# Performance work log

Hardware: AMD Instinct MI355X
Metric: run time of the kernel (lower is better)

## Reference

```python
import jax, jax.numpy as jnp
import numpy as np

B, SQ, SK, D, H = 4, 2048, 2048, 1024, 16
HD = D // H


def setup_inputs() -> dict:
    key = jax.random.key(0)
    ks = jax.random.split(key, 8)
    s = 1.0 / np.sqrt(D)
    return {
        "query": jax.random.normal(ks[0], (B, SQ, D), jnp.float32),
        "key_value": jax.random.normal(ks[1], (B, SK, D), jnp.float32),
        "Wq": jax.random.normal(ks[2], (D, D), jnp.float32) * s,
        "bq": jnp.zeros((D,), jnp.float32),
        "Wkv": jax.random.normal(ks[3], (D, 2 * D), jnp.float32) * s,
        "bkv": jnp.zeros((2 * D,), jnp.float32),
        "Wo": jax.random.normal(ks[4], (D, D), jnp.float32) * s,
        "bo": jnp.zeros((D,), jnp.float32),
    }


def reference(query, key_value, Wq, bq, Wkv, bkv, Wo, bo):
    b, sq, _ = query.shape
    sk = key_value.shape[1]
    # Q projection -> [b, H, sq, HD]
    Q = (query @ Wq + bq).reshape(b, sq, H, HD).transpose(0, 2, 1, 3)
    # fused KV projection -> [b, sk, 2, H, HD]
    KV = (key_value @ Wkv + bkv).reshape(b, sk, 2, H, HD)
    K = KV[:, :, 0].transpose(0, 2, 1, 3)  # [b, H, sk, HD]
    V = KV[:, :, 1].transpose(0, 2, 1, 3)
    scale = 1.0 / np.sqrt(HD).astype(np.float32)
    scores = jnp.einsum("bhqd,bhkd->bhqk", Q, K) * scale
    attn = jax.nn.softmax(scores, axis=-1)  # dropout is identity in eval / p=0
    out = jnp.einsum("bhqk,bhkd->bhqd", attn, V)
    out = out.transpose(0, 2, 1, 3).reshape(b, sq, D)
    return out @ Wo + bo
```

## Files before the change

kernel.cpp:

```cpp
#include <hip/hip_runtime.h>
#include <hip/hip_bf16.h>
#include <stdint.h>


typedef __bf16 bf16_t;
typedef __bf16 bf16x8 __attribute__((ext_vector_type(8)));
typedef __bf16 bf16x4 __attribute__((ext_vector_type(4)));
typedef short  s16x4  __attribute__((ext_vector_type(4)));
typedef float  f32x4  __attribute__((ext_vector_type(4)));

#define MFMA16x32(a, b, c) __builtin_amdgcn_mfma_f32_16x16x32_bf16((a), (b), (c), 0, 0, 0)

__device__ __forceinline__ f32x4 mfma16x16(bf16x4 a, bf16x4 b, f32x4 c) {
#if __has_builtin(__builtin_amdgcn_mfma_f32_16x16x16_bf16)
    return __builtin_amdgcn_mfma_f32_16x16x16_bf16(a, b, c, 0, 0, 0);
#else
    return __builtin_amdgcn_mfma_f32_16x16x16bf16_1k(
        __builtin_bit_cast(s16x4, a), __builtin_bit_cast(s16x4, b), c, 0, 0, 0);
#endif
}

__device__ __forceinline__ float fast_exp2(float x) {
#if __has_builtin(__builtin_amdgcn_exp2f)
    return __builtin_amdgcn_exp2f(x);
#else
    return exp2f(x);
#endif
}

__device__ __forceinline__ void gload16(const void* g, const void* l) {
    __builtin_amdgcn_global_load_lds(
        (__attribute__((address_space(1))) void*)(uintptr_t)g,
        (__attribute__((address_space(3))) void*)(uintptr_t)l,
        16, 0, 0);
}

#define ATTN_SCALE 0.18033688011112042f

__global__ void cvt_bf16(const float* __restrict__ in, bf16_t* __restrict__ out, int n) {
    int i = (blockIdx.x * 256 + threadIdx.x) * 8;
    if (i + 8 <= n) {
        const float4* p = (const float4*)(in + i);
        float4 a = p[0], c = p[1];
        bf16x8 v;
        v[0] = (bf16_t)a.x; v[1] = (bf16_t)a.y; v[2] = (bf16_t)a.z; v[3] = (bf16_t)a.w;
        v[4] = (bf16_t)c.x; v[5] = (bf16_t)c.y; v[6] = (bf16_t)c.z; v[7] = (bf16_t)c.w;
        *(bf16x8*)(out + i) = v;
    }
}

__global__ void transpose_cvt(const float* __restrict__ W, bf16_t* __restrict__ WT,
                              int K, int N) {
    __shared__ float tile[64][65];
    const int t = threadIdx.x;
    const int n0 = blockIdx.x * 64, k0 = blockIdx.y * 64;
#pragma unroll
    for (int i = 0; i < 16; ++i) {
        int idx = i * 256 + t;
        int r = idx >> 6, c = idx & 63;
        tile[r][c] = W[(size_t)(k0 + r) * N + n0 + c];
    }
    __syncthreads();
#pragma unroll
    for (int i = 0; i < 16; ++i) {
        int idx = i * 256 + t;
        int r = idx >> 6, c = idx & 63;
        WT[(size_t)(n0 + r) * K + k0 + c] = (bf16_t)tile[c][r];
    }
}

template <int MODE>
__global__ __launch_bounds__(256, 3)
void gemm_bt(const bf16_t* __restrict__ A, const bf16_t* __restrict__ BT,
             const float* __restrict__ bias, void* __restrict__ out0,
             void* __restrict__ out1, int M, int N, int K) {
    __shared__ __align__(16) bf16_t sA[128 * 32];
    __shared__ __align__(16) bf16_t sB[128 * 32];
    const int tid  = threadIdx.x;
    const int lane = tid & 63, w = tid >> 6;
    const int wr = w >> 1, wc = w & 1;
    const int quad = lane >> 4, l15 = lane & 15;
    const int row0 = blockIdx.y * 128, col0 = blockIdx.x * 128;

    f32x4 acc[4][4];
    const f32x4 fz = {0.f, 0.f, 0.f, 0.f};
#pragma unroll
    for (int m = 0; m < 4; ++m)
#pragma unroll
        for (int n = 0; n < 4; ++n) acc[m][n] = fz;

    for (int kt = 0; kt < K; kt += 32) {
#pragma unroll
        for (int i = 0; i < 2; ++i) {
            int c = i * 256 + tid;
            int r = c >> 2, cr = c & 3;
            gload16(A + (size_t)(row0 + r) * K + kt + cr * 8,
                    (const char*)sA + i * 4096 + w * 1024);
            gload16(BT + (size_t)(col0 + r) * K + kt + cr * 8,
                    (const char*)sB + i * 4096 + w * 1024);
        }
        __syncthreads();

        bf16x8 af[4], bfr[4];
#pragma unroll
        for (int m = 0; m < 4; ++m)
            af[m] = *(const bf16x8*)(sA + (wr * 64 + m * 16 + l15) * 32 + quad * 8);
#pragma unroll
        for (int n = 0; n < 4; ++n)
            bfr[n] = *(const bf16x8*)(sB + (wc * 64 + n * 16 + l15) * 32 + quad * 8);
#pragma unroll
        for (int m = 0; m < 4; ++m)
#pragma unroll
            for (int n = 0; n < 4; ++n)
                acc[m][n] = MFMA16x32(af[m], bfr[n], acc[m][n]);
        __syncthreads();
    }

#pragma unroll
    for (int m = 0; m < 4; ++m) {
        int rg_base = row0 + wr * 64 + m * 16 + quad * 4;
#pragma unroll
        for (int n = 0; n < 4; ++n) {
            int cg = col0 + wc * 64 + n * 16 + l15;
            float bv = bias[cg];
#pragma unroll
            for (int r = 0; r < 4; ++r) {
                int rg = rg_base + r;
                float v = acc[m][n][r] + bv;
                if constexpr (MODE == 2) {
                    ((float*)out0)[(size_t)rg * N + cg] = v;
                } else if constexpr (MODE == 0) {
                    v *= ATTN_SCALE;
                    int bb = rg >> 11, sq = rg & 2047;
                    int hh = cg >> 6, hd = cg & 63;
                    ((bf16_t*)out0)[(((size_t)(bb * 16 + hh) * 2048 + sq) << 6) | hd] =
                        (bf16_t)v;
                } else {
                    int bb = rg >> 11, sk = rg & 2047;
                    int kv = cg >> 10, j = cg & 1023;
                    int hh = j >> 6, hd = j & 63;
                    if (kv == 0)
                        ((bf16_t*)out0)[(((size_t)(bb * 16 + hh) * 2048 + sk) << 6) | hd] =
                            (bf16_t)v;
                    else
                        ((bf16_t*)out1)[(((size_t)(bb * 16 + hh) * 64 + hd) << 11) | sk] =
                            (bf16_t)v;
                }
            }
        }
    }
}

__global__ __launch_bounds__(256, 3)
void attn_kernel(const bf16_t* __restrict__ Qp, const bf16_t* __restrict__ Kb,
                 const bf16_t* __restrict__ Vt, bf16_t* __restrict__ Ob) {
    __shared__ __align__(16) char pool[40960];
    bf16_t* sQ   = (bf16_t*)pool;
    float*  redO = (float*)pool;
    float*  redL = (float*)(pool + 32768);

    const int tid = threadIdx.x;
    const int lane = tid & 63, w = tid >> 6;
    const int quad = lane >> 4, l15 = lane & 15;
    const int qt = blockIdx.x, h = blockIdx.y, b = blockIdx.z;
    const size_t bh = (size_t)b * 16 + h;

    const bf16_t* Qg = Qp + bh * (2048 * 64) + (size_t)qt * (64 * 64);
    const bf16_t* Kg = Kb + bh * (2048 * 64);
    const bf16_t* Vg = Vt + bh * (64 * 2048);

    const int srow = w * 16 + (lane >> 2);
    const int soff = (lane & 3) * 8;

#pragma unroll
    for (int hh = 0; hh < 2; ++hh) {
        gload16(Qg + srow * 64 + hh * 32 + soff, pool + hh * 4096 + w * 1024);
        gload16(Kg + srow * 64 + hh * 32 + soff, pool + 8192 + hh * 4096 + w * 1024);
        gload16(Vg + (size_t)srow * 2048 + hh * 32 + soff,
                pool + 24576 + hh * 4096 + w * 1024);
    }
    __syncthreads();

    bf16x8 qf[4][2];
#pragma unroll
    for (int qb = 0; qb < 4; ++qb)
#pragma unroll
        for (int hh = 0; hh < 2; ++hh)
            qf[qb][hh] = *(const bf16x8*)(sQ + hh * 2048 + (qb * 16 + l15) * 32 + quad * 8);

    const f32x4 fz = {0.f, 0.f, 0.f, 0.f};
    f32x4 o_[4][4];
#pragma unroll
    for (int qb = 0; qb < 4; ++qb)
#pragma unroll
        for (int nh = 0; nh < 4; ++nh) o_[qb][nh] = fz;
    float lsum[4] = {0.f, 0.f, 0.f, 0.f};

    for (int t = 0; t < 32; ++t) {
        if (t < 31) {
            const bf16_t* Kt = Kg + (size_t)(t + 1) * (64 * 64);
            char* kb_ = pool + 8192 + ((t + 1) & 1) * 8192;
            char* vb_ = pool + 24576 + ((t + 1) & 1) * 8192;
#pragma unroll
            for (int hh = 0; hh < 2; ++hh) {
                gload16(Kt + srow * 64 + hh * 32 + soff, kb_ + hh * 4096 + w * 1024);
                gload16(Vg + (size_t)srow * 2048 + (t + 1) * 64 + hh * 32 + soff,
                        vb_ + hh * 4096 + w * 1024);
            }
        }
        const bf16_t* k0 = (const bf16_t*)(pool + 8192 + (t & 1) * 8192);
        const bf16_t* v0 = (const bf16_t*)(pool + 24576 + (t & 1) * 8192);

        bf16x8 kf0 = *(const bf16x8*)(k0 + (w * 16 + l15) * 32 + quad * 8);
        bf16x8 kf1 = *(const bf16x8*)(k0 + 2048 + (w * 16 + l15) * 32 + quad * 8);

        f32x4 s[4];
#pragma unroll
        for (int qb = 0; qb < 4; ++qb) {
            s[qb] = MFMA16x32(kf0, qf[qb][0], fz);
            s[qb] = MFMA16x32(kf1, qf[qb][1], s[qb]);
        }

        bf16x4 pf[4];
#pragma unroll
        for (int qb = 0; qb < 4; ++qb) {
            float p0 = fast_exp2(s[qb][0]);
            float p1 = fast_exp2(s[qb][1]);
            float p2 = fast_exp2(s[qb][2]);
            float p3 = fast_exp2(s[qb][3]);
            lsum[qb] += (p0 + p1) + (p2 + p3);
            bf16x4 pv = {(bf16_t)p0, (bf16_t)p1, (bf16_t)p2, (bf16_t)p3};
            pf[qb] = pv;
        }

        const bf16_t* vbase = v0 + (w >> 1) * 2048 + (w & 1) * 16 + quad * 4;
#pragma unroll
        for (int nh = 0; nh < 4; ++nh) {
            bf16x4 vf = *(const bf16x4*)(vbase + (nh * 16 + l15) * 32);
#pragma unroll
            for (int qb = 0; qb < 4; ++qb)
                o_[qb][nh] = mfma16x16(pf[qb], vf, o_[qb][nh]);
        }
        __syncthreads();
    }

#pragma unroll
    for (int qb = 0; qb < 4; ++qb) {
        lsum[qb] += __shfl_xor(lsum[qb], 16);
        lsum[qb] += __shfl_xor(lsum[qb], 32);
    }
    if (quad == 0) {
#pragma unroll
        for (int qb = 0; qb < 4; ++qb) redL[w * 64 + qb * 16 + l15] = lsum[qb];
    }

    const int cq = tid >> 2;
    const int chb = (tid & 3) * 8;
    const size_t orow = (size_t)b * 2048 + (size_t)qt * 64 + cq;

#pragma unroll
    for (int ph = 0; ph < 2; ++ph) {
        __syncthreads();
#pragma unroll
        for (int qb = 0; qb < 4; ++qb)
#pragma unroll
            for (int nj = 0; nj < 2; ++nj) {
                int nh = ph * 2 + nj;
#pragma unroll
                for (int r = 0; r < 4; ++r)
                    redO[w * 2048 + (qb * 16 + quad * 4 + r) * 32 + nj * 16 + l15] =
                        o_[qb][nh][r];
            }
        __syncthreads();

        float lt = redL[cq] + redL[64 + cq] + redL[128 + cq] + redL[192 + cq];
        float linv = 1.f / lt;
        float4 a0 = {0, 0, 0, 0}, a1 = {0, 0, 0, 0};
#pragma unroll
        for (int ww = 0; ww < 4; ++ww) {
            const float4* p = (const float4*)(redO + ww * 2048 + cq * 32 + chb);
            float4 x = p[0], y = p[1];
            a0.x += x.x; a0.y += x.y; a0.z += x.z; a0.w += x.w;
            a1.x += y.x; a1.y += y.y; a1.z += y.z; a1.w += y.w;
        }
        bf16x8 ov;
        ov[0] = (bf16_t)(a0.x * linv); ov[1] = (bf16_t)(a0.y * linv);
        ov[2] = (bf16_t)(a0.z * linv); ov[3] = (bf16_t)(a0.w * linv);
        ov[4] = (bf16_t)(a1.x * linv); ov[5] = (bf16_t)(a1.y * linv);
        ov[6] = (bf16_t)(a1.z * linv); ov[7] = (bf16_t)(a1.w * linv);
        *(bf16x8*)(Ob + orow * 1024 + h * 64 + ph * 32 + chb) = ov;
    }
}

extern "C" void kernel_launch(void* const* d_in, const int* in_sizes, int n_in,
                              void* d_out, int out_size, void* d_ws, size_t ws_size,
                              hipStream_t stream) {
    const float* query     = (const float*)d_in[0];
    const float* key_value = (const float*)d_in[1];
    const float* Wq  = (const float*)d_in[2];
    const float* bq  = (const float*)d_in[3];
    const float* Wkv = (const float*)d_in[4];
    const float* bkv = (const float*)d_in[5];
    const float* Wo  = (const float*)d_in[6];
    const float* bo  = (const float*)d_in[7];
    float* out = (float*)d_out;

    char* ws = (char*)d_ws;
    const size_t MB = 1024 * 1024;
    bf16_t* WqT  = (bf16_t*)(ws + 0 * MB);
    bf16_t* WkvT = (bf16_t*)(ws + 2 * MB);
    bf16_t* WoT  = (bf16_t*)(ws + 6 * MB);
    bf16_t* qb   = (bf16_t*)(ws + 8 * MB);
    bf16_t* kvb  = (bf16_t*)(ws + 24 * MB);
    bf16_t* Qp   = (bf16_t*)(ws + 40 * MB);
    bf16_t* Kb   = (bf16_t*)(ws + 56 * MB);
    bf16_t* Vt   = (bf16_t*)(ws + 72 * MB);
    bf16_t* Ob   = (bf16_t*)(ws + 88 * MB);

    cvt_bf16<<<4096, 256, 0, stream>>>(query, qb, 8192 * 1024);
    cvt_bf16<<<4096, 256, 0, stream>>>(key_value, kvb, 8192 * 1024);
    transpose_cvt<<<dim3(16, 16), 256, 0, stream>>>(Wq, WqT, 1024, 1024);
    transpose_cvt<<<dim3(32, 16), 256, 0, stream>>>(Wkv, WkvT, 1024, 2048);
    transpose_cvt<<<dim3(16, 16), 256, 0, stream>>>(Wo, WoT, 1024, 1024);

    gemm_bt<0><<<dim3(8, 64), 256, 0, stream>>>(qb, WqT, bq, Qp, nullptr,
                                                8192, 1024, 1024);
    gemm_bt<1><<<dim3(16, 64), 256, 0, stream>>>(kvb, WkvT, bkv, Kb, Vt,
                                                 8192, 2048, 1024);
    attn_kernel<<<dim3(32, 16, 4), 256, 0, stream>>>(Qp, Kb, Vt, Ob);
    gemm_bt<2><<<dim3(8, 64), 256, 0, stream>>>(Ob, WoT, bo, out, nullptr,
                                                8192, 1024, 1024);
}
```

Measured before the change: 368.8 us.

## Swizzle LDS layouts in GEMM and attention, merge prep kernel launches

```diff
diff --git a/kernel.cpp b/kernel.cpp
--- a/kernel.cpp
+++ b/kernel.cpp
@@ -37,20 +37,33 @@
 
 #define ATTN_SCALE 0.18033688011112042f
 
-__global__ void cvt_bf16(const float* __restrict__ in, bf16_t* __restrict__ out, int n) {
-    int i = (blockIdx.x * 256 + threadIdx.x) * 8;
-    if (i + 8 <= n) {
-        const float4* p = (const float4*)(in + i);
-        float4 a = p[0], c = p[1];
-        bf16x8 v;
-        v[0] = (bf16_t)a.x; v[1] = (bf16_t)a.y; v[2] = (bf16_t)a.z; v[3] = (bf16_t)a.w;
-        v[4] = (bf16_t)c.x; v[5] = (bf16_t)c.y; v[6] = (bf16_t)c.z; v[7] = (bf16_t)c.w;
-        *(bf16x8*)(out + i) = v;
-    }
-}
-
-__global__ void transpose_cvt(const float* __restrict__ W, bf16_t* __restrict__ WT,
-                              int K, int N) {
+__global__ void cvt_bf16_2(const float* __restrict__ a, const float* __restrict__ b,
+                           bf16_t* __restrict__ oa, bf16_t* __restrict__ ob) {
+    int bid = blockIdx.x;
+    const float* in;
+    bf16_t* out;
+    if (bid < 4096) { in = a; out = oa; }
+    else            { in = b; out = ob; bid -= 4096; }
+    int i = (bid * 256 + threadIdx.x) * 8;
+    const float4* p = (const float4*)(in + i);
+    float4 x = p[0], y = p[1];
+    bf16x8 v;
+    v[0] = (bf16_t)x.x; v[1] = (bf16_t)x.y; v[2] = (bf16_t)x.z; v[3] = (bf16_t)x.w;
+    v[4] = (bf16_t)y.x; v[5] = (bf16_t)y.y; v[6] = (bf16_t)y.z; v[7] = (bf16_t)y.w;
+    *(bf16x8*)(out + i) = v;
+}
+
+__global__ void transpose_cvt3(const float* __restrict__ Wq, const float* __restrict__ Wkv,
+                               const float* __restrict__ Wo, bf16_t* __restrict__ WqT,
+                               bf16_t* __restrict__ WkvT, bf16_t* __restrict__ WoT) {
+    const float* W;
+    bf16_t* WT;
+    int N;
+    if (blockIdx.z == 0)      { W = Wq;  WT = WqT;  N = 1024; }
+    else if (blockIdx.z == 1) { W = Wkv; WT = WkvT; N = 2048; }
+    else                      { W = Wo;  WT = WoT;  N = 1024; }
+    if ((int)blockIdx.x * 64 >= N) return;
+    const int K = 1024;
     __shared__ float tile[64][65];
     const int t = threadIdx.x;
     const int n0 = blockIdx.x * 64, k0 = blockIdx.y * 64;
@@ -80,6 +93,7 @@
     const int lane = tid & 63, w = tid >> 6;
     const int wr = w >> 1, wc = w & 1;
     const int quad = lane >> 4, l15 = lane & 15;
+    const int x3 = l15 & 3;
     const int row0 = blockIdx.y * 128, col0 = blockIdx.x * 128;
 
     f32x4 acc[4][4];
@@ -94,9 +108,10 @@
         for (int i = 0; i < 2; ++i) {
             int c = i * 256 + tid;
             int r = c >> 2, cr = c & 3;
-            gload16(A + (size_t)(row0 + r) * K + kt + cr * 8,
+            int g = cr ^ (r & 3);
+            gload16(A + (size_t)(row0 + r) * K + kt + g * 8,
                     (const char*)sA + i * 4096 + w * 1024);
-            gload16(BT + (size_t)(col0 + r) * K + kt + cr * 8,
+            gload16(BT + (size_t)(col0 + r) * K + kt + g * 8,
                     (const char*)sB + i * 4096 + w * 1024);
         }
         __syncthreads();
@@ -104,10 +119,10 @@
         bf16x8 af[4], bfr[4];
 #pragma unroll
         for (int m = 0; m < 4; ++m)
-            af[m] = *(const bf16x8*)(sA + (wr * 64 + m * 16 + l15) * 32 + quad * 8);
+            af[m] = *(const bf16x8*)(sA + (wr * 64 + m * 16 + l15) * 32 + (quad ^ x3) * 8);
 #pragma unroll
         for (int n = 0; n < 4; ++n)
-            bfr[n] = *(const bf16x8*)(sB + (wc * 64 + n * 16 + l15) * 32 + quad * 8);
+            bfr[n] = *(const bf16x8*)(sB + (wc * 64 + n * 16 + l15) * 32 + (quad ^ x3) * 8);
 #pragma unroll
         for (int m = 0; m < 4; ++m)
 #pragma unroll
@@ -162,6 +177,7 @@
     const int tid = threadIdx.x;
     const int lane = tid & 63, w = tid >> 6;
     const int quad = lane >> 4, l15 = lane & 15;
+    const int x7 = l15 & 7;
     const int qt = blockIdx.x, h = blockIdx.y, b = blockIdx.z;
     const size_t bh = (size_t)b * 16 + h;
 
@@ -169,15 +185,15 @@
     const bf16_t* Kg = Kb + bh * (2048 * 64);
     const bf16_t* Vg = Vt + bh * (64 * 2048);
 
-    const int srow = w * 16 + (lane >> 2);
-    const int soff = (lane & 3) * 8;
+    const int srow = tid >> 3;
+    const int sg   = (tid & 7) ^ (srow & 7);
 
 #pragma unroll
     for (int hh = 0; hh < 2; ++hh) {
-        gload16(Qg + srow * 64 + hh * 32 + soff, pool + hh * 4096 + w * 1024);
-        gload16(Kg + srow * 64 + hh * 32 + soff, pool + 8192 + hh * 4096 + w * 1024);
-        gload16(Vg + (size_t)srow * 2048 + hh * 32 + soff,
-                pool + 24576 + hh * 4096 + w * 1024);
+        int row = hh * 32 + srow;
+        gload16(Qg + (size_t)row * 64 + sg * 8, pool + hh * 4096 + w * 1024);
+        gload16(Kg + (size_t)row * 64 + sg * 8, pool + 8192 + hh * 4096 + w * 1024);
+        gload16(Vg + (size_t)row * 2048 + sg * 8, pool + 24576 + hh * 4096 + w * 1024);
     }
     __syncthreads();
 
@@ -186,7 +202,8 @@
     for (int qb = 0; qb < 4; ++qb)
 #pragma unroll
         for (int hh = 0; hh < 2; ++hh)
-            qf[qb][hh] = *(const bf16x8*)(sQ + hh * 2048 + (qb * 16 + l15) * 32 + quad * 8);
+            qf[qb][hh] = *(const bf16x8*)(sQ + (qb * 16 + l15) * 64 +
+                                          ((hh * 4 + quad) ^ x7) * 8);
 
     const f32x4 fz = {0.f, 0.f, 0.f, 0.f};
     f32x4 o_[4][4];
@@ -203,16 +220,18 @@
             char* vb_ = pool + 24576 + ((t + 1) & 1) * 8192;
 #pragma unroll
             for (int hh = 0; hh < 2; ++hh) {
-                gload16(Kt + srow * 64 + hh * 32 + soff, kb_ + hh * 4096 + w * 1024);
-                gload16(Vg + (size_t)srow * 2048 + (t + 1) * 64 + hh * 32 + soff,
+                int row = hh * 32 + srow;
+                gload16(Kt + (size_t)row * 64 + sg * 8, kb_ + hh * 4096 + w * 1024);
+                gload16(Vg + (size_t)row * 2048 + (t + 1) * 64 + sg * 8,
                         vb_ + hh * 4096 + w * 1024);
             }
         }
         const bf16_t* k0 = (const bf16_t*)(pool + 8192 + (t & 1) * 8192);
         const bf16_t* v0 = (const bf16_t*)(pool + 24576 + (t & 1) * 8192);
 
-        bf16x8 kf0 = *(const bf16x8*)(k0 + (w * 16 + l15) * 32 + quad * 8);
-        bf16x8 kf1 = *(const bf16x8*)(k0 + 2048 + (w * 16 + l15) * 32 + quad * 8);
+        const bf16_t* krow = k0 + (w * 16 + l15) * 64;
+        bf16x8 kf0 = *(const bf16x8*)(krow + (quad ^ x7) * 8);
+        bf16x8 kf1 = *(const bf16x8*)(krow + ((quad + 4) ^ x7) * 8);
 
         f32x4 s[4];
 #pragma unroll
@@ -233,10 +252,11 @@
             pf[qb] = pv;
         }
 
-        const bf16_t* vbase = v0 + (w >> 1) * 2048 + (w & 1) * 16 + quad * 4;
+        const int vslot = (2 * w + (quad >> 1)) ^ x7;
+        const int vsub  = (quad & 1) * 4;
 #pragma unroll
         for (int nh = 0; nh < 4; ++nh) {
-            bf16x4 vf = *(const bf16x4*)(vbase + (nh * 16 + l15) * 32);
+            bf16x4 vf = *(const bf16x4*)(v0 + (nh * 16 + l15) * 64 + vslot * 8 + vsub);
 #pragma unroll
             for (int qb = 0; qb < 4; ++qb)
                 o_[qb][nh] = mfma16x16(pf[qb], vf, o_[qb][nh]);
@@ -317,11 +337,8 @@
     bf16_t* Vt   = (bf16_t*)(ws + 72 * MB);
     bf16_t* Ob   = (bf16_t*)(ws + 88 * MB);
 
-    cvt_bf16<<<4096, 256, 0, stream>>>(query, qb, 8192 * 1024);
-    cvt_bf16<<<4096, 256, 0, stream>>>(key_value, kvb, 8192 * 1024);
-    transpose_cvt<<<dim3(16, 16), 256, 0, stream>>>(Wq, WqT, 1024, 1024);
-    transpose_cvt<<<dim3(32, 16), 256, 0, stream>>>(Wkv, WkvT, 1024, 2048);
-    transpose_cvt<<<dim3(16, 16), 256, 0, stream>>>(Wo, WoT, 1024, 1024);
+    cvt_bf16_2<<<8192, 256, 0, stream>>>(query, key_value, qb, kvb);
+    transpose_cvt3<<<dim3(32, 16, 3), 256, 0, stream>>>(Wq, Wkv, Wo, WqT, WkvT, WoT);
 
     gemm_bt<0><<<dim3(8, 64), 256, 0, stream>>>(qb, WqT, bq, Qp, nullptr,
                                                 8192, 1024, 1024);
```

Result: faster. 350.2 us (-5.1%).
